# Performance work log

Measured on AMD Instinct MI355X. Metric: run time of the kernel, lower is better.

The kernel has to match this reference:

```python
import jax, jax.numpy as jnp
import numpy as np

# Domain bounds and training nu-range (from init_kwargs)
X_MIN, X_MAX = -1.0, 1.0
Y_MIN, Y_MAX = -1.0, 1.0
T_MIN, T_MAX = 0.0, 1.0
NU_MIN, NU_MAX = 0.01, 0.1

LAYERS = [4, 256, 256, 256, 256, 2]
N = 16384  # collocation points


def setup_inputs() -> dict:
    key = jax.random.key(0)
    ks = jax.random.split(key, 4 + 2 * (len(LAYERS) - 1))
    inp = {
        'x': jax.random.uniform(ks[0], (N, 1), minval=X_MIN, maxval=X_MAX, dtype=jnp.float32),
        'y': jax.random.uniform(ks[1], (N, 1), minval=Y_MIN, maxval=Y_MAX, dtype=jnp.float32),
        't': jax.random.uniform(ks[2], (N, 1), minval=T_MIN, maxval=T_MAX, dtype=jnp.float32),
        'nu': jax.random.uniform(ks[3], (N, 1), minval=NU_MIN, maxval=NU_MAX, dtype=jnp.float32),
    }
    # glorot_normal weights, zero biases (keras Dense defaults)
    for i in range(len(LAYERS) - 1):
        fan_in, fan_out = LAYERS[i], LAYERS[i + 1]
        std = (2.0 / (fan_in + fan_out)) ** 0.5
        inp[f'W{i}'] = std * jax.random.normal(ks[4 + 2 * i], (fan_in, fan_out), dtype=jnp.float32)
        inp[f'b{i}'] = jnp.zeros((fan_out,), dtype=jnp.float32)
    return inp


def _net(pt, nu, params):
    """MLP forward for a single point. pt: (3,) = (x, y, t); nu: scalar. Returns (2,) = (u, v)."""
    x, y, t = pt[0], pt[1], pt[2]
    h = jnp.stack([
        2.0 * (x - X_MIN) / (X_MAX - X_MIN) - 1.0,
        2.0 * (y - Y_MIN) / (Y_MAX - Y_MIN) - 1.0,
        2.0 * (t - T_MIN) / (T_MAX - T_MIN) - 1.0,
        2.0 * (nu - NU_MIN) / (NU_MAX - NU_MIN) - 1.0,
    ])
    for W, b in params[:-1]:
        z = h @ W + b
        h = z * jax.nn.sigmoid(z)  # swish
    W, b = params[-1]
    return h @ W + b


def _residual_point(pt, nu, params):
    """Burgers PDE residual (f_u, f_v) at one collocation point via nested forward-mode AD."""
    f = lambda p: _net(p, nu, params)
    uv = f(pt)                          # (2,)
    J = jax.jacfwd(f)(pt)               # (2,3): d(u,v)/d(x,y,t)
    H = jax.jacfwd(jax.jacfwd(f))(pt)   # (2,3,3)
    u, v = uv[0], uv[1]
    u_x, u_y, u_t = J[0, 0], J[0, 1], J[0, 2]
    v_x, v_y, v_t = J[1, 0], J[1, 1], J[1, 2]
    u_xx, u_yy = H[0, 0, 0], H[0, 1, 1]
    v_xx, v_yy = H[1, 0, 0], H[1, 1, 1]
    f_u = u_t + u * u_x + v * u_y - nu * (u_xx + u_yy)
    f_v = v_t + u * v_x + v * v_y - nu * (v_xx + v_yy)
    return jnp.stack([f_u, f_v])


def reference(x, y, t, nu, W0, b0, W1, b1, W2, b2, W3, b3, W4, b4):
    params = [(W0, b0), (W1, b1), (W2, b2), (W3, b3), (W4, b4)]
    pts = jnp.concatenate([x, y, t], axis=1)  # (N, 3)
    res = jax.vmap(lambda p, n: _residual_point(p, n, params))(pts, nu[:, 0])
    return res  # (N, 2) = [f_u, f_v]
```

## Files before the change

kernel.cpp:

```cpp
#include <hip/hip_runtime.h>

typedef _Float16 f16;
typedef _Float16 v8hf __attribute__((ext_vector_type(8)));
typedef _Float16 v4hf __attribute__((ext_vector_type(4)));
typedef _Float16 v2hf __attribute__((ext_vector_type(2)));
typedef float    v4f  __attribute__((ext_vector_type(4)));

#define NPTS 16384
#define PTS  8
#define NLAYER_ELEMS 65536

__device__ __forceinline__ int swz(int m, int j) {
    return m * 256 + ((((j >> 3) ^ (m & 7)) << 3) | (j & 7));
}

__global__ void pack_weights(const float* __restrict__ W1, const float* __restrict__ W2,
                             const float* __restrict__ W3, f16* __restrict__ bh,
                             f16* __restrict__ bl) {
    const int L = blockIdx.x >> 3, ks = blockIdx.x & 7, n = threadIdx.x;
    const float* W = (L == 0) ? W1 : (L == 1) ? W2 : W3;
    f16 h[32], l[32];
    #pragma unroll
    for (int kk = 0; kk < 32; ++kk) {
        float w = W[(ks * 32 + kk) * 256 + n];
        f16 hh = (f16)w;
        h[kk] = hh;
        l[kk] = (f16)(w - (float)hh);
    }
    size_t off = (size_t)L * NLAYER_ELEMS + (size_t)(ks * 256 + n) * 32;
    #pragma unroll
    for (int i = 0; i < 4; ++i) {
        *(v8hf*)(bh + off + 8 * i) = *(v8hf*)(h + 8 * i);
        *(v8hf*)(bl + off + 8 * i) = *(v8hf*)(l + 8 * i);
    }
}

__global__ __launch_bounds__(256, 3) void pinn_burgers_kernel(
    const float* __restrict__ gx, const float* __restrict__ gy,
    const float* __restrict__ gt, const float* __restrict__ gnu,
    const float* __restrict__ W0, const float* __restrict__ b0,
    const float* __restrict__ b1, const float* __restrict__ b2,
    const float* __restrict__ b3,
    const float* __restrict__ W4, const float* __restrict__ b4,
    const f16* __restrict__ bh, const f16* __restrict__ bl,
    float* __restrict__ out)
{
    __shared__ f16 Ah[48 * 256];
    __shared__ f16 Al[48 * 256];
    __shared__ float red[PTS][12];
    __shared__ float pin[4][PTS];

    const int tid  = threadIdx.x;
    const int lane = tid & 63;
    const int wv   = tid >> 6;
    const int ln   = lane & 15;
    const int quad = lane >> 4;
    const int lnx  = ln & 7;
    const int p0   = blockIdx.x * PTS;

    if (tid < 4 * PTS) {
        int c = tid >> 3, p = tid & 7;
        const float* src = (c == 0) ? gx : (c == 1) ? gy : (c == 2) ? gt : gnu;
        pin[c][p] = src[p0 + p];
    }
    __syncthreads();

    const int l5 = lane & 31;
    const int j0 = wv * 64 + l5 * 2;
    const int ph = (lane >> 5) * 4;

    {
        float w00[2], w01[2], w02[2], w03[2], bb[2];
        #pragma unroll
        for (int e = 0; e < 2; ++e) {
            int j = j0 + e;
            w00[e] = W0[j]; w01[e] = W0[256 + j]; w02[e] = W0[512 + j]; w03[e] = W0[768 + j];
            bb[e] = b0[j];
        }
        #pragma unroll
        for (int pp = 0; pp < 4; ++pp) {
            int p = ph + pp;
            float hx = pin[0][p];
            float hy = pin[1][p];
            float ht = 2.f * pin[2][p] - 1.f;
            float hn = 2.f * (pin[3][p] - 0.01f) * (1.f / 0.09f) - 1.f;
            float a[6][2];
            #pragma unroll
            for (int e = 0; e < 2; ++e) {
                float z  = hx * w00[e] + hy * w01[e] + ht * w02[e] + hn * w03[e] + bb[e];
                float zx = w00[e], zy = w01[e], zt = 2.f * w02[e];
                float s  = 1.f / (1.f + __expf(-z));
                float g1 = s + z * s * (1.f - s);
                float g2 = s * (1.f - s) * (2.f + z * (1.f - 2.f * s));
                a[0][e] = z * s;
                a[1][e] = g1 * zx; a[2][e] = g1 * zy; a[3][e] = g1 * zt;
                a[4][e] = g2 * zx * zx; a[5][e] = g2 * zy * zy;
            }
            #pragma unroll
            for (int c = 0; c < 6; ++c) {
                int idx = swz(c * PTS + p, j0);
                v2hf hh = { (f16)a[c][0], (f16)a[c][1] };
                v2hf ll = { (f16)(a[c][0] - (float)hh[0]), (f16)(a[c][1] - (float)hh[1]) };
                *(v2hf*)&Ah[idx] = hh;
                *(v2hf*)&Al[idx] = ll;
            }
        }
    }
    __syncthreads();

    const float* bias_ptr[3] = { b1, b2, b3 };
    for (int L = 0; L < 3; ++L) {
        const f16* __restrict__ bhL = bh + (size_t)L * NLAYER_ELEMS;
        const f16* __restrict__ blL = bl + (size_t)L * NLAYER_ELEMS;
        const float* __restrict__ bv = bias_ptr[L];

        v4f acc[4][3];
        #pragma unroll
        for (int t = 0; t < 4; ++t)
            #pragma unroll
            for (int mt = 0; mt < 3; ++mt)
                acc[t][mt] = (v4f){0.f, 0.f, 0.f, 0.f};

        #pragma unroll 2
        for (int ks = 0; ks < 8; ++ks) {
            const int cb = (((4 * ks + quad) ^ lnx) << 3);
            v8hf a_h[3], a_l[3];
            #pragma unroll
            for (int mt = 0; mt < 3; ++mt) {
                const int rb = (mt * 16 + ln) * 256 + cb;
                a_h[mt] = *(const v8hf*)&Ah[rb];
                a_l[mt] = *(const v8hf*)&Al[rb];
            }
            v8hf w_h[4], w_l[4];
            #pragma unroll
            for (int t = 0; t < 4; ++t) {
                int n = wv * 64 + t * 16 + ln;
                size_t o = (size_t)(ks * 256 + n) * 32 + quad * 8;
                w_h[t] = *(const v8hf*)(bhL + o);
                w_l[t] = *(const v8hf*)(blL + o);
            }
            #pragma unroll
            for (int t = 0; t < 4; ++t)
                #pragma unroll
                for (int mt = 0; mt < 3; ++mt) {
                    acc[t][mt] = __builtin_amdgcn_mfma_f32_16x16x32_f16(w_h[t], a_h[mt], acc[t][mt], 0, 0, 0);
                    acc[t][mt] = __builtin_amdgcn_mfma_f32_16x16x32_f16(w_h[t], a_l[mt], acc[t][mt], 0, 0, 0);
                    acc[t][mt] = __builtin_amdgcn_mfma_f32_16x16x32_f16(w_l[t], a_h[mt], acc[t][mt], 0, 0, 0);
                }
        }
        __syncthreads();

        #pragma unroll
        for (int t = 0; t < 4; ++t)
            #pragma unroll
            for (int mt = 0; mt < 3; ++mt) {
                v4f a = acc[t][mt];
                int nb = wv * 64 + t * 16 + quad * 4;
                int m  = mt * 16 + ln;
                if (mt == 0 && ln < PTS) {
                    const float4 bq = *(const float4*)(bv + nb);
                    a[0] += bq.x; a[1] += bq.y; a[2] += bq.z; a[3] += bq.w;
                }
                v4hf hi = { (f16)a[0], (f16)a[1], (f16)a[2], (f16)a[3] };
                v4hf lo = { (f16)(a[0] - (float)hi[0]), (f16)(a[1] - (float)hi[1]),
                            (f16)(a[2] - (float)hi[2]), (f16)(a[3] - (float)hi[3]) };
                int idx = swz(m, nb);
                *(v4hf*)&Ah[idx] = hi;
                *(v4hf*)&Al[idx] = lo;
            }

        {
            #pragma unroll
            for (int pp = 0; pp < 4; ++pp) {
                int p = ph + pp;
                float z[6][2];
                #pragma unroll
                for (int c = 0; c < 6; ++c) {
                    int idx = swz(c * PTS + p, j0);
                    v2hf hh = *(v2hf*)&Ah[idx];
                    v2hf ll = *(v2hf*)&Al[idx];
                    z[c][0] = (float)hh[0] + (float)ll[0];
                    z[c][1] = (float)hh[1] + (float)ll[1];
                }
                float a[6][2];
                #pragma unroll
                for (int e = 0; e < 2; ++e) {
                    float zz = z[0][e];
                    float s  = 1.f / (1.f + __expf(-zz));
                    float g1 = s + zz * s * (1.f - s);
                    float g2 = s * (1.f - s) * (2.f + zz * (1.f - 2.f * s));
                    a[0][e] = zz * s;
                    a[1][e] = g1 * z[1][e];
                    a[2][e] = g1 * z[2][e];
                    a[3][e] = g1 * z[3][e];
                    a[4][e] = g2 * z[1][e] * z[1][e] + g1 * z[4][e];
                    a[5][e] = g2 * z[2][e] * z[2][e] + g1 * z[5][e];
                }
                #pragma unroll
                for (int c = 0; c < 6; ++c) {
                    int idx = swz(c * PTS + p, j0);
                    v2hf hh = { (f16)a[c][0], (f16)a[c][1] };
                    v2hf ll = { (f16)(a[c][0] - (float)hh[0]), (f16)(a[c][1] - (float)hh[1]) };
                    *(v2hf*)&Ah[idx] = hh;
                    *(v2hf*)&Al[idx] = ll;
                }
            }
        }
        __syncthreads();
    }

    #pragma unroll
    for (int d = 0; d < 24; ++d) {
        int D  = wv * 24 + d;
        int p  = D / 12;
        int rm = D % 12;
        int c  = rm >> 1;
        int o  = rm & 1;
        int m  = c * PTS + p;
        int k0 = lane * 4;
        int idx = swz(m, k0);
        v4hf hh = *(v4hf*)&Ah[idx];
        v4hf ll = *(v4hf*)&Al[idx];
        float partial = 0.f;
        #pragma unroll
        for (int i = 0; i < 4; ++i)
            partial += ((float)hh[i] + (float)ll[i]) * W4[(k0 + i) * 2 + o];
        #pragma unroll
        for (int off = 32; off > 0; off >>= 1)
            partial += __shfl_down(partial, off);
        if (lane == 0)
            red[p][rm] = partial + ((c == 0) ? b4[o] : 0.f);
    }
    __syncthreads();

    if (tid < PTS) {
        int p = tid;
        float u   = red[p][0],  v   = red[p][1];
        float ux  = red[p][2],  vx  = red[p][3];
        float uy  = red[p][4],  vy  = red[p][5];
        float ut  = red[p][6],  vt  = red[p][7];
        float uxx = red[p][8],  vxx = red[p][9];
        float uyy = red[p][10], vyy = red[p][11];
        float nuv = pin[3][p];
        float fu = ut + u * ux + v * uy - nuv * (uxx + uyy);
        float fv = vt + u * vx + v * vy - nuv * (vxx + vyy);
        out[(p0 + p) * 2 + 0] = fu;
        out[(p0 + p) * 2 + 1] = fv;
    }
}

extern "C" void kernel_launch(void* const* d_in, const int* in_sizes, int n_in,
                              void* d_out, int out_size, void* d_ws, size_t ws_size,
                              hipStream_t stream) {
    const float* x  = (const float*)d_in[0];
    const float* y  = (const float*)d_in[1];
    const float* t  = (const float*)d_in[2];
    const float* nu = (const float*)d_in[3];
    const float* W0 = (const float*)d_in[4];
    const float* b0 = (const float*)d_in[5];
    const float* W1 = (const float*)d_in[6];
    const float* b1 = (const float*)d_in[7];
    const float* W2 = (const float*)d_in[8];
    const float* b2 = (const float*)d_in[9];
    const float* W3 = (const float*)d_in[10];
    const float* b3 = (const float*)d_in[11];
    const float* W4 = (const float*)d_in[12];
    const float* b4 = (const float*)d_in[13];
    float* o = (float*)d_out;

    f16* bh = (f16*)d_ws;
    f16* bl = bh + 3 * (size_t)NLAYER_ELEMS;

    hipLaunchKernelGGL(pack_weights, dim3(24), dim3(256), 0, stream, W1, W2, W3, bh, bl);
    hipLaunchKernelGGL(pinn_burgers_kernel, dim3(NPTS / PTS), dim3(256), 0, stream,
                       x, y, t, nu, W0, b0, b1, b2, b3, W4, b4, bh, bl, o);
}
```

Before: 228.4 us.

## Store GEMM outputs as raw fp32 halves and vectorize activation stages to 8-wide

The MFMA epilogue no longer splits fp32 values into f16 hi/lo pairs. It writes the raw 32-bit words as two 16-bit halves through byte permutes, and the activation stage reconstructs the floats losslessly. The activation and input-layer stages now give each lane 8 contiguous neurons of one point, using 16-byte LDS accesses and vectorized W0 loads. The last layer's activation output is stored raw for the fp32 output reduction. This cuts conversion ALU work and LDS instruction count, at the cost of more registers per lane.

```diff
diff --git a/kernel.cpp b/kernel.cpp
--- a/kernel.cpp
+++ b/kernel.cpp
@@ -12,6 +12,19 @@
 
 __device__ __forceinline__ int swz(int m, int j) {
     return m * 256 + ((((j >> 3) ^ (m & 7)) << 3) | (j & 7));
+}
+
+__device__ __forceinline__ uint32_t pk_lo(float x0, float x1) {
+    return __builtin_amdgcn_perm(__float_as_uint(x1), __float_as_uint(x0), 0x05040100u);
+}
+__device__ __forceinline__ uint32_t pk_hi(float x0, float x1) {
+    return __builtin_amdgcn_perm(__float_as_uint(x1), __float_as_uint(x0), 0x07060302u);
+}
+__device__ __forceinline__ float up0(uint32_t lo, uint32_t hi) {
+    return __uint_as_float(__builtin_amdgcn_perm(hi, lo, 0x05040100u));
+}
+__device__ __forceinline__ float up1(uint32_t lo, uint32_t hi) {
+    return __uint_as_float(__builtin_amdgcn_perm(hi, lo, 0x07060302u));
 }
 
 __global__ void pack_weights(const float* __restrict__ W1, const float* __restrict__ W2,
@@ -65,46 +78,65 @@
     }
     __syncthreads();
 
-    const int l5 = lane & 31;
-    const int j0 = wv * 64 + l5 * 2;
-    const int ph = (lane >> 5) * 4;
+    const int pa    = lane >> 3;
+    const int jb    = lane & 7;
+    const int jbase = wv * 64 + jb * 8;
+
+    auto store_split = [&](const float (&A)[8], int c) {
+        v8hf hh, ll;
+        #pragma unroll
+        for (int e = 0; e < 8; ++e) {
+            f16 hv = (f16)A[e];
+            hh[e] = hv;
+            ll[e] = (f16)(A[e] - (float)hv);
+        }
+        int idx = swz(c * PTS + pa, jbase);
+        *(v8hf*)&Ah[idx] = hh;
+        *(v8hf*)&Al[idx] = ll;
+    };
+    auto store_raw = [&](const float (&A)[8], int c) {
+        uint4 lo, hi;
+        lo.x = pk_lo(A[0], A[1]); lo.y = pk_lo(A[2], A[3]);
+        lo.z = pk_lo(A[4], A[5]); lo.w = pk_lo(A[6], A[7]);
+        hi.x = pk_hi(A[0], A[1]); hi.y = pk_hi(A[2], A[3]);
+        hi.z = pk_hi(A[4], A[5]); hi.w = pk_hi(A[6], A[7]);
+        int idx = swz(c * PTS + pa, jbase);
+        *(uint4*)&Ah[idx] = lo;
+        *(uint4*)&Al[idx] = hi;
+    };
 
     {
-        float w00[2], w01[2], w02[2], w03[2], bb[2];
-        #pragma unroll
-        for (int e = 0; e < 2; ++e) {
-            int j = j0 + e;
-            w00[e] = W0[j]; w01[e] = W0[256 + j]; w02[e] = W0[512 + j]; w03[e] = W0[768 + j];
-            bb[e] = b0[j];
-        }
-        #pragma unroll
-        for (int pp = 0; pp < 4; ++pp) {
-            int p = ph + pp;
-            float hx = pin[0][p];
-            float hy = pin[1][p];
-            float ht = 2.f * pin[2][p] - 1.f;
-            float hn = 2.f * (pin[3][p] - 0.01f) * (1.f / 0.09f) - 1.f;
-            float a[6][2];
-            #pragma unroll
-            for (int e = 0; e < 2; ++e) {
-                float z  = hx * w00[e] + hy * w01[e] + ht * w02[e] + hn * w03[e] + bb[e];
-                float zx = w00[e], zy = w01[e], zt = 2.f * w02[e];
-                float s  = 1.f / (1.f + __expf(-z));
-                float g1 = s + z * s * (1.f - s);
-                float g2 = s * (1.f - s) * (2.f + z * (1.f - 2.f * s));
-                a[0][e] = z * s;
-                a[1][e] = g1 * zx; a[2][e] = g1 * zy; a[3][e] = g1 * zt;
-                a[4][e] = g2 * zx * zx; a[5][e] = g2 * zy * zy;
-            }
-            #pragma unroll
-            for (int c = 0; c < 6; ++c) {
-                int idx = swz(c * PTS + p, j0);
-                v2hf hh = { (f16)a[c][0], (f16)a[c][1] };
-                v2hf ll = { (f16)(a[c][0] - (float)hh[0]), (f16)(a[c][1] - (float)hh[1]) };
-                *(v2hf*)&Ah[idx] = hh;
-                *(v2hf*)&Al[idx] = ll;
-            }
-        }
+        v4f w0v[2], w1v[2], w2v[2], w3v[2], bbv[2];
+        #pragma unroll
+        for (int h = 0; h < 2; ++h) {
+            w0v[h] = *(const v4f*)(W0 +   0 + jbase + 4 * h);
+            w1v[h] = *(const v4f*)(W0 + 256 + jbase + 4 * h);
+            w2v[h] = *(const v4f*)(W0 + 512 + jbase + 4 * h);
+            w3v[h] = *(const v4f*)(W0 + 768 + jbase + 4 * h);
+            bbv[h] = *(const v4f*)(b0 + jbase + 4 * h);
+        }
+        float hx = pin[0][pa];
+        float hy = pin[1][pa];
+        float ht = 2.f * pin[2][pa] - 1.f;
+        float hn = 2.f * (pin[3][pa] - 0.01f) * (1.f / 0.09f) - 1.f;
+        float A0[8], A1[8], A2[8], A3[8], A4[8], A5[8];
+        #pragma unroll
+        for (int e = 0; e < 8; ++e) {
+            float w0 = w0v[e >> 2][e & 3];
+            float w1 = w1v[e >> 2][e & 3];
+            float w2 = w2v[e >> 2][e & 3];
+            float w3 = w3v[e >> 2][e & 3];
+            float z  = hx * w0 + hy * w1 + ht * w2 + hn * w3 + bbv[e >> 2][e & 3];
+            float zx = w0, zy = w1, zt = 2.f * w2;
+            float s  = 1.f / (1.f + __expf(-z));
+            float g1 = s * (1.f + z * (1.f - s));
+            float g2 = s * (1.f - s) * (2.f + z * (1.f - 2.f * s));
+            A0[e] = z * s;
+            A1[e] = g1 * zx; A2[e] = g1 * zy; A3[e] = g1 * zt;
+            A4[e] = g2 * zx * zx; A5[e] = g2 * zy * zy;
+        }
+        store_split(A0, 0); store_split(A1, 1); store_split(A2, 2);
+        store_split(A3, 3); store_split(A4, 4); store_split(A5, 5);
     }
     __syncthreads();
 
@@ -161,49 +193,52 @@
                     const float4 bq = *(const float4*)(bv + nb);
                     a[0] += bq.x; a[1] += bq.y; a[2] += bq.z; a[3] += bq.w;
                 }
-                v4hf hi = { (f16)a[0], (f16)a[1], (f16)a[2], (f16)a[3] };
-                v4hf lo = { (f16)(a[0] - (float)hi[0]), (f16)(a[1] - (float)hi[1]),
-                            (f16)(a[2] - (float)hi[2]), (f16)(a[3] - (float)hi[3]) };
                 int idx = swz(m, nb);
-                *(v4hf*)&Ah[idx] = hi;
-                *(v4hf*)&Al[idx] = lo;
+                uint2 lo, hi;
+                lo.x = pk_lo(a[0], a[1]); lo.y = pk_lo(a[2], a[3]);
+                hi.x = pk_hi(a[0], a[1]); hi.y = pk_hi(a[2], a[3]);
+                *(uint2*)&Ah[idx] = lo;
+                *(uint2*)&Al[idx] = hi;
             }
 
         {
-            #pragma unroll
-            for (int pp = 0; pp < 4; ++pp) {
-                int p = ph + pp;
-                float z[6][2];
-                #pragma unroll
-                for (int c = 0; c < 6; ++c) {
-                    int idx = swz(c * PTS + p, j0);
-                    v2hf hh = *(v2hf*)&Ah[idx];
-                    v2hf ll = *(v2hf*)&Al[idx];
-                    z[c][0] = (float)hh[0] + (float)ll[0];
-                    z[c][1] = (float)hh[1] + (float)ll[1];
-                }
-                float a[6][2];
-                #pragma unroll
-                for (int e = 0; e < 2; ++e) {
-                    float zz = z[0][e];
-                    float s  = 1.f / (1.f + __expf(-zz));
-                    float g1 = s + zz * s * (1.f - s);
-                    float g2 = s * (1.f - s) * (2.f + zz * (1.f - 2.f * s));
-                    a[0][e] = zz * s;
-                    a[1][e] = g1 * z[1][e];
-                    a[2][e] = g1 * z[2][e];
-                    a[3][e] = g1 * z[3][e];
-                    a[4][e] = g2 * z[1][e] * z[1][e] + g1 * z[4][e];
-                    a[5][e] = g2 * z[2][e] * z[2][e] + g1 * z[5][e];
-                }
-                #pragma unroll
-                for (int c = 0; c < 6; ++c) {
-                    int idx = swz(c * PTS + p, j0);
-                    v2hf hh = { (f16)a[c][0], (f16)a[c][1] };
-                    v2hf ll = { (f16)(a[c][0] - (float)hh[0]), (f16)(a[c][1] - (float)hh[1]) };
-                    *(v2hf*)&Ah[idx] = hh;
-                    *(v2hf*)&Al[idx] = ll;
-                }
+            float z0[8], z1[8], z2[8], z3[8], z4[8], z5[8];
+            auto load_z = [&](float (&Z)[8], int c) {
+                int idx = swz(c * PTS + pa, jbase);
+                uint4 lo = *(const uint4*)&Ah[idx];
+                uint4 hi = *(const uint4*)&Al[idx];
+                Z[0] = up0(lo.x, hi.x); Z[1] = up1(lo.x, hi.x);
+                Z[2] = up0(lo.y, hi.y); Z[3] = up1(lo.y, hi.y);
+                Z[4] = up0(lo.z, hi.z); Z[5] = up1(lo.z, hi.z);
+                Z[6] = up0(lo.w, hi.w); Z[7] = up1(lo.w, hi.w);
+            };
+            load_z(z0, 0); load_z(z1, 1); load_z(z2, 2);
+            load_z(z3, 3); load_z(z4, 4); load_z(z5, 5);
+
+            float A0[8], g1[8], g2[8];
+            #pragma unroll
+            for (int e = 0; e < 8; ++e) {
+                float zz = z0[e];
+                float s  = 1.f / (1.f + __expf(-zz));
+                A0[e] = zz * s;
+                g1[e] = s * (1.f + zz * (1.f - s));
+                g2[e] = s * (1.f - s) * (2.f + zz * (1.f - 2.f * s));
+            }
+            float A1[8], A2[8], A3[8], A4[8], A5[8];
+            #pragma unroll
+            for (int e = 0; e < 8; ++e) {
+                A1[e] = g1[e] * z1[e];
+                A2[e] = g1[e] * z2[e];
+                A3[e] = g1[e] * z3[e];
+                A4[e] = g2[e] * z1[e] * z1[e] + g1[e] * z4[e];
+                A5[e] = g2[e] * z2[e] * z2[e] + g1[e] * z5[e];
+            }
+            if (L < 2) {
+                store_split(A0, 0); store_split(A1, 1); store_split(A2, 2);
+                store_split(A3, 3); store_split(A4, 4); store_split(A5, 5);
+            } else {
+                store_raw(A0, 0); store_raw(A1, 1); store_raw(A2, 2);
+                store_raw(A3, 3); store_raw(A4, 4); store_raw(A5, 5);
             }
         }
         __syncthreads();
@@ -219,12 +254,12 @@
         int m  = c * PTS + p;
         int k0 = lane * 4;
         int idx = swz(m, k0);
-        v4hf hh = *(v4hf*)&Ah[idx];
-        v4hf ll = *(v4hf*)&Al[idx];
-        float partial = 0.f;
-        #pragma unroll
-        for (int i = 0; i < 4; ++i)
-            partial += ((float)hh[i] + (float)ll[i]) * W4[(k0 + i) * 2 + o];
+        uint2 lo = *(const uint2*)&Ah[idx];
+        uint2 hi = *(const uint2*)&Al[idx];
+        float h0 = up0(lo.x, hi.x), h1 = up1(lo.x, hi.x);
+        float h2 = up0(lo.y, hi.y), h3 = up1(lo.y, hi.y);
+        float partial = h0 * W4[(k0 + 0) * 2 + o] + h1 * W4[(k0 + 1) * 2 + o]
+                      + h2 * W4[(k0 + 2) * 2 + o] + h3 * W4[(k0 + 3) * 2 + o];
         #pragma unroll
         for (int off = 32; off > 0; off >>= 1)
             partial += __shfl_down(partial, off);
```

Result: faster. 219.2 us (-4.0%).
